# Optimization experiments

Hardware: AMD Instinct MI355X
Metric: run time of the kernel (lower is better)

## Reference

```python
import jax, jax.numpy as jnp
import numpy as np

NEG_SLOPE = 0.2  # PyG GATConv default

def gat_layer(x, src, dst, W, a_src, a_dst, b, N):
    # h = W x  (PyG applies linear before attention)
    h = x @ W                                   # [N, hid]
    al_src = h @ a_src                          # [N]
    al_dst = h @ a_dst                          # [N]
    e = jax.nn.leaky_relu(al_src[src] + al_dst[dst], NEG_SLOPE)  # [E]
    # segment softmax over incoming edges of each destination node
    m = jax.ops.segment_max(e, dst, num_segments=N)
    e = jnp.exp(e - m[dst])
    s = jax.ops.segment_sum(e, dst, num_segments=N)
    coef = e / s[dst]                           # [E]
    out = jax.ops.segment_sum(h[src] * coef[:, None], dst, num_segments=N)
    return out + b

def setup_inputs() -> dict:
    key = jax.random.key(0)
    ks = jax.random.split(key, 12)
    N, E, in_dim, hid, out_dim, G = 100000, 1600000, 128, 64, 1, 256
    x = jax.random.normal(ks[0], (N, in_dim), dtype=jnp.float32)
    edge_index = jax.random.randint(ks[1], (2, E), 0, N, dtype=jnp.int64)
    batch = jnp.sort(jax.random.randint(ks[2], (N,), 0, G, dtype=jnp.int64))
    def glorot(k, shape):
        lim = float(np.sqrt(6.0 / (shape[0] + shape[-1])))
        return jax.random.uniform(k, shape, jnp.float32, -lim, lim)
    return {
        "x": x, "edge_index": edge_index, "batch": batch,
        "W1": glorot(ks[3], (in_dim, hid)),
        "a_src1": glorot(ks[4], (hid,)), "a_dst1": glorot(ks[5], (hid,)),
        "b1": jnp.zeros((hid,), jnp.float32),
        "W2": glorot(ks[6], (hid, hid)),
        "a_src2": glorot(ks[7], (hid,)), "a_dst2": glorot(ks[8], (hid,)),
        "b2": jnp.zeros((hid,), jnp.float32),
        "Wfc": glorot(ks[9], (hid, out_dim)),
        "bfc": jnp.zeros((out_dim,), jnp.float32),
    }

def reference(x, edge_index, batch, W1, a_src1, a_dst1, b1, W2, a_src2, a_dst2, b2, Wfc, bfc):
    N = x.shape[0]
    G = 256  # number of graphs in the batch
    # add self-loops (PyG GATConv default add_self_loops=True)
    loops = jnp.arange(N, dtype=edge_index.dtype)
    src = jnp.concatenate([edge_index[0], loops])
    dst = jnp.concatenate([edge_index[1], loops])
    h = jax.nn.elu(gat_layer(x, src, dst, W1, a_src1, a_dst1, b1, N))
    h = jax.nn.elu(gat_layer(h, src, dst, W2, a_src2, a_dst2, b2, N))
    # global mean pool over graph ids
    sums = jax.ops.segment_sum(h, batch, num_segments=G)
    cnts = jax.ops.segment_sum(jnp.ones((N,), h.dtype), batch, num_segments=G)
    pooled = sums / jnp.maximum(cnts, 1.0)[:, None]
    return pooled @ Wfc + bfc
```

## Files before the change

kernel.cpp:

```cpp
#include <hip/hip_runtime.h>
#include <hip/hip_bf16.h>
#include <cstdint>


#define BIN_SHIFT 8
#define BIN_NODES 256
#define BIN_CAP 6144
#define PLACE_CHUNK 2048

__device__ __forceinline__ float wave_reduce_sum(float v) {
#pragma unroll
  for (int off = 32; off > 0; off >>= 1) v += __shfl_xor(v, off, 64);
  return v;
}

__device__ __forceinline__ unsigned short f2bf(float f) {
  unsigned int u = __float_as_uint(f);
  u += 0x7fffu + ((u >> 16) & 1u);
  return (unsigned short)(u >> 16);
}
__device__ __forceinline__ float bf2f(unsigned short u) {
  return __uint_as_float(((unsigned int)u) << 16);
}


__global__ __launch_bounds__(256) void bin_place_kernel(
    const int* __restrict__ ei, int E, int M, int NB,
    int* __restrict__ binCursor, unsigned int* __restrict__ binned) {
  __shared__ int cur[512];
  __shared__ int res[512];
  const int t = threadIdx.x;
  const int cbase = blockIdx.x * PLACE_CHUNK;

  for (int i = t; i < NB; i += 256) cur[i] = 0;
  __syncthreads();

  unsigned int pk[PLACE_CHUNK / 256];
  int br[PLACE_CHUNK / 256];
#pragma unroll
  for (int j = 0; j < PLACE_CHUNK / 256; ++j) {
    int i = cbase + t + j * 256;
    if (i < M) {
      int s, d;
      if (i < E) { s = ei[i]; d = ei[E + i]; } else { s = d = i - E; }
      int b = d >> BIN_SHIFT;
      int r = atomicAdd(&cur[b], 1);
      pk[j] = ((unsigned int)(d & (BIN_NODES - 1)) << 24) | (unsigned int)s;
      br[j] = (b << 16) | r;
    } else {
      br[j] = -1;
    }
  }
  __syncthreads();
  for (int i = t; i < NB; i += 256) {
    int c = cur[i];
    res[i] = c ? atomicAdd(&binCursor[i], c) : 0;
  }
  __syncthreads();
#pragma unroll
  for (int j = 0; j < PLACE_CHUNK / 256; ++j) {
    if (br[j] >= 0) {
      int b = br[j] >> 16;
      int pos = res[b] + (br[j] & 0xFFFF);
      if (pos < BIN_CAP) binned[(size_t)b * BIN_CAP + pos] = pk[j];
    }
  }
}

__global__ __launch_bounds__(256) void csr_finalize_kernel(
    const unsigned int* __restrict__ binned, const int* __restrict__ binCursor,
    int* __restrict__ rowbeg, int* __restrict__ rowend, int* __restrict__ csrc,
    int N, int NB) {
  __shared__ int cnt[256];
  __shared__ int off[256];
  __shared__ int wsum[4];
  const int b = blockIdx.x;
  const int t = threadIdx.x;
  const int nodeBase = b << BIN_SHIFT;
  const int eBase = b * BIN_CAP;
  const int cntE = binCursor[b];

  cnt[t] = 0;
  __syncthreads();
  for (int i = t; i < cntE; i += 256) {
    atomicAdd(&cnt[binned[eBase + i] >> 24], 1);
  }
  __syncthreads();
  int v = cnt[t];
  {
    int lane = t & 63, wv = t >> 6;
    int x = v;
#pragma unroll
    for (int o = 1; o < 64; o <<= 1) {
      int u = __shfl_up(x, o, 64);
      if (lane >= o) x += u;
    }
    if (lane == 63) wsum[wv] = x;
    __syncthreads();
    int woff = 0;
    for (int j = 0; j < wv; j++) woff += wsum[j];
    off[t] = woff + x - v;
  }
  __syncthreads();
  int node = nodeBase + t;
  if (node < N) {
    rowbeg[node] = eBase + off[t];
    rowend[node] = eBase + off[t] + v;
  }
  cnt[t] = off[t];
  __syncthreads();
  for (int i = t; i < cntE; i += 256) {
    unsigned int pk = binned[eBase + i];
    int r = atomicAdd(&cnt[pk >> 24], 1);
    csrc[eBase + r] = (int)(pk & 0xFFFFFFu);
  }
}

__global__ void bounds_kernel(const int* __restrict__ batch, int* __restrict__ gstart,
                              int N, int G) {
  int g = blockIdx.x * blockDim.x + threadIdx.x;
  if (g > G) return;
  int lo = 0, hi = N;
  while (lo < hi) {
    int mid = (lo + hi) >> 1;
    if (batch[mid] < g) lo = mid + 1;
    else hi = mid;
  }
  gstart[g] = lo;
}


template <int KDIM>
__global__ __launch_bounds__(256) void gemm64(const float* __restrict__ A,
                                              const float* __restrict__ W,
                                              unsigned short* __restrict__ hb,
                                              const float* __restrict__ a_src,
                                              const float* __restrict__ a_dst,
                                              float* __restrict__ alsrc,
                                              float* __restrict__ aldst, int N) {
  __shared__ float As[32][68];
  __shared__ float Ws[32][68];
  const int block_m = blockIdx.x * 64;
  const int t = threadIdx.x;
  const int tc = t & 15;
  const int tr = t >> 4;
  const int c0 = tc * 4, r0 = tr * 4;
  float acc[4][4] = {};

  for (int kc = 0; kc < KDIM; kc += 32) {
    for (int q = t; q < 512; q += 256) {
      int node = q >> 3, f4 = q & 7;
      int gn = block_m + node;
      if (gn >= N) gn = N - 1;
      const float4 v = *(const float4*)(A + (size_t)gn * KDIM + kc + f4 * 4);
      As[f4 * 4 + 0][node] = v.x;
      As[f4 * 4 + 1][node] = v.y;
      As[f4 * 4 + 2][node] = v.z;
      As[f4 * 4 + 3][node] = v.w;
    }
    for (int q = t; q < 512; q += 256) {
      int k = q >> 4, f4 = q & 15;
      const float4 v = *(const float4*)(W + (size_t)(kc + k) * 64 + f4 * 4);
      *(float4*)&Ws[k][f4 * 4] = v;
    }
    __syncthreads();
#pragma unroll
    for (int k = 0; k < 32; ++k) {
      float4 a = *(const float4*)&As[k][r0];
      float4 b = *(const float4*)&Ws[k][c0];
      acc[0][0] += a.x * b.x; acc[0][1] += a.x * b.y; acc[0][2] += a.x * b.z; acc[0][3] += a.x * b.w;
      acc[1][0] += a.y * b.x; acc[1][1] += a.y * b.y; acc[1][2] += a.y * b.z; acc[1][3] += a.y * b.w;
      acc[2][0] += a.z * b.x; acc[2][1] += a.z * b.y; acc[2][2] += a.z * b.z; acc[2][3] += a.z * b.w;
      acc[3][0] += a.w * b.x; acc[3][1] += a.w * b.y; acc[3][2] += a.w * b.z; acc[3][3] += a.w * b.w;
    }
    __syncthreads();
  }

  const float as0 = a_src[c0], as1 = a_src[c0 + 1], as2 = a_src[c0 + 2], as3 = a_src[c0 + 3];
  const float ad0 = a_dst[c0], ad1 = a_dst[c0 + 1], ad2 = a_dst[c0 + 2], ad3 = a_dst[c0 + 3];
#pragma unroll
  for (int i = 0; i < 4; ++i) {
    int gn = block_m + r0 + i;
    if (gn < N) {
      ushort4 u;
      u.x = f2bf(acc[i][0]); u.y = f2bf(acc[i][1]);
      u.z = f2bf(acc[i][2]); u.w = f2bf(acc[i][3]);
      *(ushort4*)(hb + (size_t)gn * 64 + c0) = u;
    }
    float ps = acc[i][0] * as0 + acc[i][1] * as1 + acc[i][2] * as2 + acc[i][3] * as3;
    float pd = acc[i][0] * ad0 + acc[i][1] * ad1 + acc[i][2] * ad2 + acc[i][3] * ad3;
#pragma unroll
    for (int off = 1; off < 16; off <<= 1) {
      ps += __shfl_xor(ps, off, 64);
      pd += __shfl_xor(pd, off, 64);
    }
    if (tc == 0 && gn < N) {
      alsrc[gn] = ps;
      aldst[gn] = pd;
    }
  }
}

template <int ELU>
__global__ __launch_bounds__(256) void spmm_fused_kernel(
    const int* __restrict__ rowbeg, const int* __restrict__ rowend,
    const int* __restrict__ csrc,
    const float* __restrict__ alsrc, const float* __restrict__ aldst,
    const unsigned short* __restrict__ hb, const float* __restrict__ bias,
    float* __restrict__ outbuf, int N) {
  const int t = threadIdx.x;
  const int l = t & 15;
  const int gb = t & 48;
  const int half = l >> 3;
  const int f0 = (l & 7) * 8;
  const int node = blockIdx.x * 16 + (t >> 4);
  if (node >= N) return;
  const int start = rowbeg[node];
  const int end = rowend[node];
  const float ad = aldst[node];

  float ssum = 0.f;
  float acc[8] = {};

  int i0 = start + l;
  bool v0 = i0 < end;
  int s = v0 ? csrc[i0] : 0;
  float w;
  {
    float e = alsrc[s] + ad;
    e = (e > 0.f) ? e : 0.2f * e;
    w = v0 ? __expf(fminf(e, 80.f)) : 0.f;
  }

  for (int base = start; base < end; base += 16) {
    int in = base + 16 + l;
    bool vn = in < end;
    int sn = vn ? csrc[in] : 0;
    float aln = alsrc[sn];

    uint4 u[8];
#pragma unroll
    for (int j = 0; j < 8; ++j) {
      int sj = __shfl(s, gb + 2 * j + half, 64);
      u[j] = *(const uint4*)(hb + (size_t)sj * 64 + f0);
    }

    ssum += w;
#pragma unroll
    for (int j = 0; j < 8; ++j) {
      float wj = __shfl(w, gb + 2 * j + half, 64);
      acc[0] += wj * __uint_as_float(u[j].x << 16);
      acc[1] += wj * __uint_as_float(u[j].x & 0xFFFF0000u);
      acc[2] += wj * __uint_as_float(u[j].y << 16);
      acc[3] += wj * __uint_as_float(u[j].y & 0xFFFF0000u);
      acc[4] += wj * __uint_as_float(u[j].z << 16);
      acc[5] += wj * __uint_as_float(u[j].z & 0xFFFF0000u);
      acc[6] += wj * __uint_as_float(u[j].w << 16);
      acc[7] += wj * __uint_as_float(u[j].w & 0xFFFF0000u);
    }

    float en = aln + ad;
    en = (en > 0.f) ? en : 0.2f * en;
    w = vn ? __expf(fminf(en, 80.f)) : 0.f;
    s = sn;
  }

#pragma unroll
  for (int k = 0; k < 8; ++k) acc[k] += __shfl_xor(acc[k], 8, 64);
#pragma unroll
  for (int off = 1; off < 16; off <<= 1) ssum += __shfl_xor(ssum, off, 64);

  if (half == 0) {
    float inv = 1.0f / ssum;
    float r[8];
#pragma unroll
    for (int k = 0; k < 8; ++k) r[k] = acc[k] * inv;
    if (ELU) {
      const float4 b40 = *(const float4*)(bias + f0);
      const float4 b41 = *(const float4*)(bias + f0 + 4);
      r[0] += b40.x; r[1] += b40.y; r[2] += b40.z; r[3] += b40.w;
      r[4] += b41.x; r[5] += b41.y; r[6] += b41.z; r[7] += b41.w;
#pragma unroll
      for (int k = 0; k < 8; ++k) r[k] = (r[k] > 0.f) ? r[k] : expm1f(r[k]);
    }
    *(float4*)(outbuf + (size_t)node * 64 + f0) = make_float4(r[0], r[1], r[2], r[3]);
    *(float4*)(outbuf + (size_t)node * 64 + f0 + 4) = make_float4(r[4], r[5], r[6], r[7]);
  }
}

__global__ __launch_bounds__(256) void post_pool_kernel(
    const float* __restrict__ acc, const float* __restrict__ bias,
    const int* __restrict__ batch, float* __restrict__ pool, int N) {
  __shared__ float4 red4[16][17];
  __shared__ int sB[16];
  __shared__ int uni;
  const int t = threadIdx.x;
  const int ln = t >> 4;
  const int f4 = t & 15;
  const int base = blockIdx.x * 16;
  const int node = base + ln;

  if (t < 16) {
    int nn = base + t;
    sB[t] = (nn < N) ? batch[nn] : -1;
  }
  __syncthreads();
  if (t == 0) {
    int u = (base + 15 < N);
    for (int i = 1; i < 16; i++) u &= (sB[i] == sB[0]);
    uni = u;
  }

  float4 v = make_float4(0.f, 0.f, 0.f, 0.f);
  if (node < N) {
    v = *(const float4*)(acc + ((size_t)node * 16 + f4) * 4);
    const float4 b4 = *(const float4*)(bias + f4 * 4);
    v.x += b4.x; v.y += b4.y; v.z += b4.z; v.w += b4.w;
    v.x = (v.x > 0.f) ? v.x : expm1f(v.x);
    v.y = (v.y > 0.f) ? v.y : expm1f(v.y);
    v.z = (v.z > 0.f) ? v.z : expm1f(v.z);
    v.w = (v.w > 0.f) ? v.w : expm1f(v.w);
  }
  red4[ln][f4] = v;
  __syncthreads();

  if (t < 64) {
    const float* rf = (const float*)red4;
    if (uni) {
      float s = 0.f;
#pragma unroll
      for (int n = 0; n < 16; n++) s += rf[n * 68 + t];
      atomicAdd(&pool[(size_t)sB[0] * 64 + t], s);
    } else {
      for (int n = 0; n < 16; n++) {
        int g = sB[n];
        if (g >= 0) atomicAdd(&pool[(size_t)g * 64 + t], rf[n * 68 + t]);
      }
    }
  }
}

__global__ void final_kernel(const float* __restrict__ pool, const int* __restrict__ gstart,
                             const float* __restrict__ Wfc, const float* __restrict__ bfc,
                             float* __restrict__ out, int G) {
  int wid = (blockIdx.x * blockDim.x + threadIdx.x) >> 6;
  int lane = threadIdx.x & 63;
  if (wid >= G) return;
  float c = (float)max(gstart[wid + 1] - gstart[wid], 1);
  float v = pool[(size_t)wid * 64 + lane] * (1.0f / c) * Wfc[lane];
  v = wave_reduce_sum(v);
  if (lane == 0) out[wid] = v + bfc[0];
}


extern "C" void kernel_launch(void* const* d_in, const int* in_sizes, int n_in,
                              void* d_out, int out_size, void* d_ws, size_t ws_size,
                              hipStream_t stream) {
  const float* x     = (const float*)d_in[0];
  const int*   ei    = (const int*)d_in[1];
  const int*   batch = (const int*)d_in[2];
  const float* W1    = (const float*)d_in[3];
  const float* asrc1 = (const float*)d_in[4];
  const float* adst1 = (const float*)d_in[5];
  const float* b1    = (const float*)d_in[6];
  const float* W2    = (const float*)d_in[7];
  const float* asrc2 = (const float*)d_in[8];
  const float* adst2 = (const float*)d_in[9];
  const float* b2    = (const float*)d_in[10];
  const float* Wfc   = (const float*)d_in[11];
  const float* bfc   = (const float*)d_in[12];
  float* out = (float*)d_out;

  const int N = in_sizes[0] / 128;
  const int E = in_sizes[1] / 2;
  const int G = 256;
  const int M = E + N;
  const int NB = (N + BIN_NODES - 1) >> BIN_SHIFT;

  char* p = (char*)d_ws;
  auto alloc = [&](size_t bytes) {
    char* r = p;
    p += (bytes + 255) & ~size_t(255);
    return r;
  };
  float*          h1e    = (float*)alloc((size_t)N * 64 * 4);
  float*          accbuf = (float*)alloc((size_t)N * 64 * 4);
  unsigned short* hb     = (unsigned short*)alloc((size_t)N * 64 * 2);
  float* alsrc  = (float*)alloc((size_t)N * 4);
  float* aldst  = (float*)alloc((size_t)N * 4);
  int*   rowbeg = (int*)alloc((size_t)N * 4);
  int*   rowend = (int*)alloc((size_t)N * 4);
  int*   csrc   = (int*)alloc((size_t)NB * BIN_CAP * 4);
  unsigned int* binned = (unsigned int*)alloc((size_t)NB * BIN_CAP * 4);
  int*   binCursor = (int*)alloc((size_t)NB * 4);
  float* pool   = (float*)alloc((size_t)G * 64 * 4);
  int*   gstart = (int*)alloc((size_t)(G + 1) * 4);

  hipMemsetAsync(binCursor, 0, (size_t)NB * 4, stream);
  bin_place_kernel<<<(M + PLACE_CHUNK - 1) / PLACE_CHUNK, 256, 0, stream>>>(
      ei, E, M, NB, binCursor, binned);
  csr_finalize_kernel<<<NB, 256, 0, stream>>>(binned, binCursor, rowbeg, rowend,
                                              csrc, N, NB);
  bounds_kernel<<<2, 256, 0, stream>>>(batch, gstart, N, G);

  gemm64<128><<<(N + 63) / 64, 256, 0, stream>>>(x, W1, hb, asrc1, adst1, alsrc, aldst, N);
  spmm_fused_kernel<1><<<(N + 15) / 16, 256, 0, stream>>>(rowbeg, rowend, csrc, alsrc,
                                                          aldst, hb, b1, h1e, N);

  gemm64<64><<<(N + 63) / 64, 256, 0, stream>>>(h1e, W2, hb, asrc2, adst2, alsrc, aldst, N);
  spmm_fused_kernel<0><<<(N + 15) / 16, 256, 0, stream>>>(rowbeg, rowend, csrc, alsrc,
                                                          aldst, hb, nullptr, accbuf, N);
  hipMemsetAsync(pool, 0, (size_t)G * 64 * 4, stream);
  post_pool_kernel<<<(N + 15) / 16, 256, 0, stream>>>(accbuf, b2, batch, pool, N);

  final_kernel<<<(G * 64 + 255) / 256, 256, 0, stream>>>(pool, gstart, Wfc, bfc, out, G);
}
```

Baseline: 300.2 us.

## Replace scalar FP32 GEMM with split-bf16 MFMA GEMM for node projections

Replaces the FP32 FMA-based 64-column GEMM with a matrix-core version that splits A and W into bf16 hi/lo parts and accumulates three MFMA products, keeping close to FP32 accuracy. A small pre-kernel splits and transposes the weights once per call. The aim is to cut the ALU cost of the two projection GEMMs. In exchange it adds two tiny launches and extra conversion work on A tiles, and the hb stores become scalar 2-byte writes.

```diff
diff --git a/kernel.cpp b/kernel.cpp
--- a/kernel.cpp
+++ b/kernel.cpp
@@ -7,6 +7,9 @@
 #define BIN_NODES 256
 #define BIN_CAP 6144
 #define PLACE_CHUNK 2048
+
+typedef __attribute__((ext_vector_type(8))) short bf16x8;
+typedef __attribute__((ext_vector_type(4))) float f32x4;
 
 __device__ __forceinline__ float wave_reduce_sum(float v) {
 #pragma unroll
@@ -130,71 +133,95 @@
 }
 
 
+__global__ void wsplit_kernel(const float* __restrict__ W, unsigned short* __restrict__ hi,
+                              unsigned short* __restrict__ lo, int K) {
+  int idx = blockIdx.x * 256 + threadIdx.x;
+  if (idx >= K * 64) return;
+  int n = idx & 63, k = idx >> 6;
+  float v = W[(size_t)k * 64 + n];
+  unsigned short h = f2bf(v);
+  hi[(size_t)n * K + k] = h;
+  lo[(size_t)n * K + k] = f2bf(v - bf2f(h));
+}
+
 template <int KDIM>
-__global__ __launch_bounds__(256) void gemm64(const float* __restrict__ A,
-                                              const float* __restrict__ W,
-                                              unsigned short* __restrict__ hb,
-                                              const float* __restrict__ a_src,
-                                              const float* __restrict__ a_dst,
-                                              float* __restrict__ alsrc,
-                                              float* __restrict__ aldst, int N) {
-  __shared__ float As[32][68];
-  __shared__ float Ws[32][68];
+__global__ __launch_bounds__(256) void gemm_mfma(
+    const float* __restrict__ A, const unsigned short* __restrict__ Wt_hi,
+    const unsigned short* __restrict__ Wt_lo, unsigned short* __restrict__ hb,
+    const float* __restrict__ a_src, const float* __restrict__ a_dst,
+    float* __restrict__ alsrc, float* __restrict__ aldst, int N) {
+  __shared__ unsigned short Ah[64][40], Al[64][40], Bh[64][40], Bl[64][40];
   const int block_m = blockIdx.x * 64;
   const int t = threadIdx.x;
-  const int tc = t & 15;
-  const int tr = t >> 4;
-  const int c0 = tc * 4, r0 = tr * 4;
-  float acc[4][4] = {};
+  const int lane = t & 63;
+  const int m0 = (t >> 6) * 16;
+  const int lc = lane & 15;
+  const int lr = lane >> 4;
+  const int srow = t >> 2;
+  const int skslot = (t & 3) * 8;
+
+  f32x4 acc[4] = {};
 
   for (int kc = 0; kc < KDIM; kc += 32) {
-    for (int q = t; q < 512; q += 256) {
-      int node = q >> 3, f4 = q & 7;
-      int gn = block_m + node;
+    {
+      int gn = block_m + srow;
       if (gn >= N) gn = N - 1;
-      const float4 v = *(const float4*)(A + (size_t)gn * KDIM + kc + f4 * 4);
-      As[f4 * 4 + 0][node] = v.x;
-      As[f4 * 4 + 1][node] = v.y;
-      As[f4 * 4 + 2][node] = v.z;
-      As[f4 * 4 + 3][node] = v.w;
-    }
-    for (int q = t; q < 512; q += 256) {
-      int k = q >> 4, f4 = q & 15;
-      const float4 v = *(const float4*)(W + (size_t)(kc + k) * 64 + f4 * 4);
-      *(float4*)&Ws[k][f4 * 4] = v;
+      const float4 v0 = *(const float4*)(A + (size_t)gn * KDIM + kc + skslot);
+      const float4 v1 = *(const float4*)(A + (size_t)gn * KDIM + kc + skslot + 4);
+      float v[8] = {v0.x, v0.y, v0.z, v0.w, v1.x, v1.y, v1.z, v1.w};
+      unsigned short h8[8], l8[8];
+#pragma unroll
+      for (int j = 0; j < 8; ++j) {
+        h8[j] = f2bf(v[j]);
+        l8[j] = f2bf(v[j] - bf2f(h8[j]));
+      }
+      *(uint4*)&Ah[srow][skslot] = *(const uint4*)h8;
+      *(uint4*)&Al[srow][skslot] = *(const uint4*)l8;
+    }
+    {
+      const uint4 wh = *(const uint4*)(Wt_hi + (size_t)srow * KDIM + kc + skslot);
+      const uint4 wl = *(const uint4*)(Wt_lo + (size_t)srow * KDIM + kc + skslot);
+      *(uint4*)&Bh[srow][skslot] = wh;
+      *(uint4*)&Bl[srow][skslot] = wl;
     }
     __syncthreads();
-#pragma unroll
-    for (int k = 0; k < 32; ++k) {
-      float4 a = *(const float4*)&As[k][r0];
-      float4 b = *(const float4*)&Ws[k][c0];
-      acc[0][0] += a.x * b.x; acc[0][1] += a.x * b.y; acc[0][2] += a.x * b.z; acc[0][3] += a.x * b.w;
-      acc[1][0] += a.y * b.x; acc[1][1] += a.y * b.y; acc[1][2] += a.y * b.z; acc[1][3] += a.y * b.w;
-      acc[2][0] += a.z * b.x; acc[2][1] += a.z * b.y; acc[2][2] += a.z * b.z; acc[2][3] += a.z * b.w;
-      acc[3][0] += a.w * b.x; acc[3][1] += a.w * b.y; acc[3][2] += a.w * b.z; acc[3][3] += a.w * b.w;
+
+    const bf16x8 ah = *(const bf16x8*)&Ah[m0 + lc][lr * 8];
+    const bf16x8 al = *(const bf16x8*)&Al[m0 + lc][lr * 8];
+#pragma unroll
+    for (int nf = 0; nf < 4; ++nf) {
+      const bf16x8 bh = *(const bf16x8*)&Bh[nf * 16 + lc][lr * 8];
+      const bf16x8 bl = *(const bf16x8*)&Bl[nf * 16 + lc][lr * 8];
+      acc[nf] = __builtin_amdgcn_mfma_f32_16x16x32_bf16(ah, bh, acc[nf], 0, 0, 0);
+      acc[nf] = __builtin_amdgcn_mfma_f32_16x16x32_bf16(ah, bl, acc[nf], 0, 0, 0);
+      acc[nf] = __builtin_amdgcn_mfma_f32_16x16x32_bf16(al, bh, acc[nf], 0, 0, 0);
     }
     __syncthreads();
   }
 
-  const float as0 = a_src[c0], as1 = a_src[c0 + 1], as2 = a_src[c0 + 2], as3 = a_src[c0 + 3];
-  const float ad0 = a_dst[c0], ad1 = a_dst[c0 + 1], ad2 = a_dst[c0 + 2], ad3 = a_dst[c0 + 3];
-#pragma unroll
-  for (int i = 0; i < 4; ++i) {
-    int gn = block_m + r0 + i;
-    if (gn < N) {
-      ushort4 u;
-      u.x = f2bf(acc[i][0]); u.y = f2bf(acc[i][1]);
-      u.z = f2bf(acc[i][2]); u.w = f2bf(acc[i][3]);
-      *(ushort4*)(hb + (size_t)gn * 64 + c0) = u;
-    }
-    float ps = acc[i][0] * as0 + acc[i][1] * as1 + acc[i][2] * as2 + acc[i][3] * as3;
-    float pd = acc[i][0] * ad0 + acc[i][1] * ad1 + acc[i][2] * ad2 + acc[i][3] * ad3;
+  float as4[4], ad4[4];
+#pragma unroll
+  for (int nf = 0; nf < 4; ++nf) {
+    as4[nf] = a_src[nf * 16 + lc];
+    ad4[nf] = a_dst[nf * 16 + lc];
+  }
+#pragma unroll
+  for (int r = 0; r < 4; ++r) {
+    const int gn = block_m + m0 + lr * 4 + r;
+    float ps = 0.f, pd = 0.f;
+#pragma unroll
+    for (int nf = 0; nf < 4; ++nf) {
+      const float v = acc[nf][r];
+      if (gn < N) hb[(size_t)gn * 64 + nf * 16 + lc] = f2bf(v);
+      ps += v * as4[nf];
+      pd += v * ad4[nf];
+    }
 #pragma unroll
     for (int off = 1; off < 16; off <<= 1) {
       ps += __shfl_xor(ps, off, 64);
       pd += __shfl_xor(pd, off, 64);
     }
-    if (tc == 0 && gn < N) {
+    if (lc == 0 && gn < N) {
       alsrc[gn] = ps;
       aldst[gn] = pd;
     }
@@ -395,6 +422,10 @@
   int*   binCursor = (int*)alloc((size_t)NB * 4);
   float* pool   = (float*)alloc((size_t)G * 64 * 4);
   int*   gstart = (int*)alloc((size_t)(G + 1) * 4);
+  unsigned short* w1thi = (unsigned short*)alloc((size_t)64 * 128 * 2);
+  unsigned short* w1tlo = (unsigned short*)alloc((size_t)64 * 128 * 2);
+  unsigned short* w2thi = (unsigned short*)alloc((size_t)64 * 64 * 2);
+  unsigned short* w2tlo = (unsigned short*)alloc((size_t)64 * 64 * 2);
 
   hipMemsetAsync(binCursor, 0, (size_t)NB * 4, stream);
   bin_place_kernel<<<(M + PLACE_CHUNK - 1) / PLACE_CHUNK, 256, 0, stream>>>(
@@ -402,12 +433,16 @@
   csr_finalize_kernel<<<NB, 256, 0, stream>>>(binned, binCursor, rowbeg, rowend,
                                               csrc, N, NB);
   bounds_kernel<<<2, 256, 0, stream>>>(batch, gstart, N, G);
-
-  gemm64<128><<<(N + 63) / 64, 256, 0, stream>>>(x, W1, hb, asrc1, adst1, alsrc, aldst, N);
+  wsplit_kernel<<<(128 * 64 + 255) / 256, 256, 0, stream>>>(W1, w1thi, w1tlo, 128);
+  wsplit_kernel<<<(64 * 64 + 255) / 256, 256, 0, stream>>>(W2, w2thi, w2tlo, 64);
+
+  gemm_mfma<128><<<(N + 63) / 64, 256, 0, stream>>>(x, w1thi, w1tlo, hb, asrc1, adst1,
+                                                    alsrc, aldst, N);
   spmm_fused_kernel<1><<<(N + 15) / 16, 256, 0, stream>>>(rowbeg, rowend, csrc, alsrc,
                                                           aldst, hb, b1, h1e, N);
 
-  gemm64<64><<<(N + 63) / 64, 256, 0, stream>>>(h1e, W2, hb, asrc2, adst2, alsrc, aldst, N);
+  gemm_mfma<64><<<(N + 63) / 64, 256, 0, stream>>>(h1e, w2thi, w2tlo, hb, asrc2, adst2,
+                                                   alsrc, aldst, N);
   spmm_fused_kernel<0><<<(N + 15) / 16, 256, 0, stream>>>(rowbeg, rowend, csrc, alsrc,
                                                           aldst, hb, nullptr, accbuf, N);
   hipMemsetAsync(pool, 0, (size_t)G * 64 * 4, stream);
```

New measurement: 279.1 us. 1.08x faster.
